# Kernel tuning notes

Measured on AMD Instinct MI355X. Metric: run time of the kernel, lower is better.

Reference implementation:

```python
import jax, jax.numpy as jnp
import numpy as np

B, C, D_IN, D_H, D_QK = 64, 512, 1024, 1024, 512
EPS = 1e-5


def setup_inputs() -> dict:
    key = jax.random.key(0)
    ks = jax.random.split(key, 24)
    din2 = D_IN + D_H  # concat([x, h]) feature dim
    s_qk = 1.0 / np.sqrt(din2)
    inp = {
        "x": jax.random.normal(ks[0], (B, C, D_IN), jnp.float32),
        "h": jax.random.normal(ks[1], (B, C, D_H), jnp.float32),
    }
    i = 2
    for g in ("r", "z", "n"):
        inp[f"Wq_{g}"] = jax.random.normal(ks[i], (din2, D_QK), jnp.float32) * s_qk; i += 1
        inp[f"bq_{g}"] = jnp.zeros((D_QK,), jnp.float32)
        inp[f"Wk_{g}"] = jax.random.normal(ks[i], (din2, D_QK), jnp.float32) * s_qk; i += 1
        inp[f"bk_{g}"] = jnp.zeros((D_QK,), jnp.float32)
        inp[f"Wv_{g}"] = jax.random.normal(ks[i], (din2, D_H), jnp.float32) * s_qk; i += 1
        inp[f"bv_{g}"] = jnp.zeros((D_H,), jnp.float32)
    inp["gamma"] = jnp.ones((D_H,), jnp.float32)
    inp["beta"] = jnp.zeros((D_H,), jnp.float32)
    return inp


def _self_attention(xin, Wq, bq, Wk, bk, Wv, bv):
    # xin: (B, C, 2D) ; attention over channel axis C
    Q = xin @ Wq + bq            # (B, C, d_qk)
    K = xin @ Wk + bk            # (B, C, d_qk)
    V = xin @ Wv + bv            # (B, C, d_h)
    scale = 1.0 / jnp.sqrt(jnp.asarray(Q.shape[-1], jnp.float32))
    scores = jnp.einsum("bcd,bed->bce", Q, K) * scale   # (B, C, C)
    attn = jax.nn.softmax(scores, axis=-1)
    return jnp.einsum("bce,bed->bcd", attn, V)          # (B, C, d_h)


def reference(x, h,
              Wq_r, bq_r, Wk_r, bk_r, Wv_r, bv_r,
              Wq_z, bq_z, Wk_z, bk_z, Wv_z, bv_z,
              Wq_n, bq_n, Wk_n, bk_n, Wv_n, bv_n,
              gamma, beta):
    xh = jnp.concatenate([x, h], axis=2)
    r = _self_attention(xh, Wq_r, bq_r, Wk_r, bk_r, Wv_r, bv_r)
    z = _self_attention(xh, Wq_z, bq_z, Wk_z, bk_z, Wv_z, bv_z)
    reset = jax.nn.sigmoid(r)
    update = jax.nn.sigmoid(z)
    xhr = jnp.concatenate([x, h * reset], axis=2)
    n = _self_attention(xhr, Wq_n, bq_n, Wk_n, bk_n, Wv_n, bv_n)
    new_state = (1.0 - update) * h + update * jnp.tanh(n)
    # LayerNorm over last dim
    mu = jnp.mean(new_state, axis=-1, keepdims=True)
    var = jnp.var(new_state, axis=-1, keepdims=True)
    return (new_state - mu) * jax.lax.rsqrt(var + EPS) * gamma + beta
```

## Files before the change

kernel.cpp:

```cpp
#include <hip/hip_runtime.h>
#include <math.h>

typedef __attribute__((ext_vector_type(8))) short short8;
typedef __attribute__((ext_vector_type(4))) float f32x4;

#define EPI_BF16   0
#define EPI_SCORES 1
#define EPI_R      2
#define EPI_Z      3
#define EPI_N      4

__device__ __forceinline__ unsigned short f2bf(float f) {
    unsigned int u = __float_as_uint(f);
    u += 0x7fffu + ((u >> 16) & 1u);
    return (unsigned short)(u >> 16);
}
__device__ __forceinline__ float bf2f(unsigned short s) {
    return __uint_as_float(((unsigned int)s) << 16);
}

struct alignas(8) us4 { unsigned short a, b, c, d; };

#define GLD_LDS16(gp, lp) \
    __builtin_amdgcn_global_load_lds((const __attribute__((address_space(1))) unsigned int*)(gp), \
                                     (__attribute__((address_space(3))) unsigned int*)(lp), 16, 0, 0)

#define BAR   do { asm volatile("" ::: "memory"); __builtin_amdgcn_s_barrier(); \
                   asm volatile("" ::: "memory"); } while (0)
#define VMC4  asm volatile("s_waitcnt vmcnt(4)" ::: "memory")
#define VMC0  asm volatile("s_waitcnt vmcnt(0)" ::: "memory")

template<int EPI, int SWZ>
__global__ void __launch_bounds__(512, 2)
gemm256(const unsigned short* __restrict__ A, long long sAb, int lda,
        const unsigned short* __restrict__ Bt, long long sBb, int ldb,
        const float* __restrict__ bias,
        void* __restrict__ C, long long sCb, int ldc,
        int K, float scale,
        const float* __restrict__ hptr,
        const unsigned short* __restrict__ updptr)
{
    extern __shared__ char smem[];

    const int z = blockIdx.z;
    A  += (size_t)z * (size_t)sAb;
    Bt += (size_t)z * (size_t)sBb;

    int bx, by;
    if (SWZ) {
        const int bid = blockIdx.y * 8 + blockIdx.x;
        const int xcd = bid & 7, i = bid >> 3;
        bx = i & 7;
        by = (xcd << 4) | (i >> 3);
    } else {
        bx = blockIdx.x; by = blockIdx.y;
    }
    const int m0 = by * 256;
    const int n0 = bx * 256;

    const int tid = threadIdx.x;
    const int w  = tid >> 6;
    const int l  = tid & 63;
    const int wr = w >> 2;
    const int wc = w & 3;
    const int lr = l & 15;
    const int lg = l >> 4;
    const int rs = (lr & 7) << 4;

    const int srw = l >> 3;
    const int scb = ((l & 7) << 4) ^ (srw << 4);

    const long long ldab = (long long)lda * 2;
    const long long ldbb = (long long)ldb * 2;

    f32x4 acc[2][4][4] = {};
    short8 a[4][2], b[4][2];

#define STAGE1(gbase, ldbytes, grow0, ldsoff) { \
    const char* g_ = (const char*)(gbase) + \
        (size_t)((grow0) + w*8 + srw) * (ldbytes) + scb; \
    GLD_LDS16(g_, smem + (ldsoff) + (w << 10)); }

#define AOFF(buf) ((buf)*65536)
#define BOFF(buf) ((buf)*65536 + 32768)

#define STAGE_A0(kt, buf) { STAGE1(A, ldab, m0 + 0   + 0*0, AOFF(buf) + 0);      \
                            STAGE1(A + (size_t)(kt)*0, ldab, m0 + 128, AOFF(buf) + 16384); } (void)0
#define STAGE_B0(kt, buf) { STAGE1(Bt, ldbb, n0 + 0,   BOFF(buf) + 0);      \
                            STAGE1(Bt, ldbb, n0 + 128, BOFF(buf) + 16384); } (void)0
#define STAGE_A1(kt, buf) { STAGE1(A, ldab, m0 + 64,  AOFF(buf) + 8192);  \
                            STAGE1(A, ldab, m0 + 192, AOFF(buf) + 24576); } (void)0
#define STAGE_B1(kt, buf) { STAGE1(Bt, ldbb, n0 + 64,  BOFF(buf) + 8192);  \
                            STAGE1(Bt, ldbb, n0 + 192, BOFF(buf) + 24576); } (void)0

#define LDA8(MH, buf) { \
    const char* Ab_ = smem + AOFF(buf); \
    _Pragma("unroll") \
    for (int mf = 0; mf < 4; ++mf) { \
        const int row_ = wr*128 + (MH)*64 + mf*16 + lr; \
        _Pragma("unroll") \
        for (int kk = 0; kk < 2; ++kk) \
            a[mf][kk] = *(const short8*)(Ab_ + row_*128 + ((kk*64 + lg*16) ^ rs)); } }

#define LDB4(BH, buf) { \
    const char* Bb_ = smem + BOFF(buf); \
    _Pragma("unroll") \
    for (int nf = 0; nf < 2; ++nf) { \
        const int row_ = wc*64 + (BH)*32 + nf*16 + lr; \
        _Pragma("unroll") \
        for (int kk = 0; kk < 2; ++kk) \
            b[(BH)*2+nf][kk] = *(const short8*)(Bb_ + row_*128 + ((kk*64 + lg*16) ^ rs)); } }

#define MMA16(MH, BH) { \
    __builtin_amdgcn_s_setprio(1); \
    _Pragma("unroll") \
    for (int kk = 0; kk < 2; ++kk) \
    _Pragma("unroll") \
    for (int mf = 0; mf < 4; ++mf) \
    _Pragma("unroll") \
    for (int nf = 0; nf < 2; ++nf) \
        acc[MH][mf][(BH)*2+nf] = __builtin_amdgcn_mfma_f32_16x16x32_bf16( \
            a[mf][kk], b[(BH)*2+nf][kk], acc[MH][mf][(BH)*2+nf], 0, 0, 0); \
    __builtin_amdgcn_s_setprio(0); }

    {
        const unsigned short* A0p = A;           const unsigned short* B0p = Bt;
        (void)A0p; (void)B0p;
        { const long long kb = 0;
          STAGE1(A  + (kb>>1), ldab, m0 + 0,   AOFF(0) + 0);
          STAGE1(A  + (kb>>1), ldab, m0 + 128, AOFF(0) + 16384);
          STAGE1(A  + (kb>>1), ldab, m0 + 64,  AOFF(0) + 8192);
          STAGE1(A  + (kb>>1), ldab, m0 + 192, AOFF(0) + 24576);
          STAGE1(Bt + (kb>>1), ldbb, n0 + 0,   BOFF(0) + 0);
          STAGE1(Bt + (kb>>1), ldbb, n0 + 128, BOFF(0) + 16384);
          STAGE1(Bt + (kb>>1), ldbb, n0 + 64,  BOFF(0) + 8192);
          STAGE1(Bt + (kb>>1), ldbb, n0 + 192, BOFF(0) + 24576); }
        { const long long kb = 128;
          STAGE1(A  + (kb>>1), ldab, m0 + 0,   AOFF(1) + 0);
          STAGE1(A  + (kb>>1), ldab, m0 + 128, AOFF(1) + 16384);
          STAGE1(A  + (kb>>1), ldab, m0 + 64,  AOFF(1) + 8192);
          STAGE1(A  + (kb>>1), ldab, m0 + 192, AOFF(1) + 24576); }
        VMC4;
        BAR;
    }

    const int NT = K >> 6;
    for (int t = 0; t < NT; ++t) {
        const int p = t & 1, q = p ^ 1;
        const unsigned short* An = A  + (size_t)(t + 2) * 64;
        const unsigned short* Bn = Bt + (size_t)(t + 1) * 64;
        const bool sB = (t + 1 < NT), sA = (t + 2 < NT);

        LDA8(0, p); LDB4(0, p);
        if (sB) { STAGE1(Bn, ldbb, n0 + 0,   BOFF(q) + 0);
                  STAGE1(Bn, ldbb, n0 + 128, BOFF(q) + 16384); }
        BAR;
        MMA16(0, 0);
        LDB4(1, p);
        if (sB) { STAGE1(Bn, ldbb, n0 + 64,  BOFF(q) + 8192);
                  STAGE1(Bn, ldbb, n0 + 192, BOFF(q) + 24576); }
        BAR;
        MMA16(0, 1);
        LDA8(1, p);
        if (sA) { STAGE1(An, ldab, m0 + 0,   AOFF(p) + 0);
                  STAGE1(An, ldab, m0 + 128, AOFF(p) + 16384); }
        BAR;
        MMA16(1, 1);
        BAR;
        if (sA) { STAGE1(An, ldab, m0 + 64,  AOFF(p) + 8192);
                  STAGE1(An, ldab, m0 + 192, AOFF(p) + 24576);
                  VMC4; }
        else if (sB) { VMC0; }
        BAR;
        MMA16(1, 0);
    }

    const int Mb = gridDim.y << 8;
    const size_t zc = (size_t)z * (size_t)sCb;
    #pragma unroll
    for (int mh = 0; mh < 2; ++mh) {
        #pragma unroll
        for (int mf = 0; mf < 4; ++mf) {
            #pragma unroll
            for (int nf = 0; nf < 4; ++nf) {
                const int col = n0 + wc * 64 + nf * 16 + lr;
                const float bval = (EPI == EPI_BF16) ? bias[col] : 0.0f;
                #pragma unroll
                for (int r = 0; r < 4; ++r) {
                    const int row = m0 + wr * 128 + mh * 64 + mf * 16 + lg * 4 + r;
                    float v = acc[mh][mf][nf][r] + bval;
                    if (EPI == EPI_BF16) {
                        ((unsigned short*)C)[zc + (size_t)row * ldc + col] = f2bf(v);
                    } else if (EPI == EPI_SCORES) {
                        ((float*)C)[zc + (size_t)row * ldc + col] = v * scale;
                    } else if (EPI == EPI_R) {
                        const size_t flat = (size_t)z * Mb + row;
                        const float hh = hptr[flat * 1024 + col];
                        const float sg = 1.0f / (1.0f + __expf(-v));
                        ((unsigned short*)C)[flat * 2048 + 1024 + col] = f2bf(hh * sg);
                    } else if (EPI == EPI_Z) {
                        const size_t flat = (size_t)z * Mb + row;
                        const float sg = 1.0f / (1.0f + __expf(-v));
                        ((unsigned short*)C)[flat * 1024 + col] = f2bf(sg);
                    } else {
                        const size_t flat = (size_t)z * Mb + row;
                        const float u  = bf2f(updptr[flat * 1024 + col]);
                        const float hh = hptr[flat * 1024 + col];
                        ((float*)C)[flat * 1024 + col] = (1.0f - u) * hh + u * tanhf(v);
                    }
                }
            }
        }
    }
#undef STAGE1
#undef AOFF
#undef BOFF
#undef STAGE_A0
#undef STAGE_A1
#undef STAGE_B0
#undef STAGE_B1
#undef LDA8
#undef LDB4
#undef MMA16
}


__global__ void __launch_bounds__(256)
prep_xh(const float* __restrict__ x, const float* __restrict__ h, unsigned short* __restrict__ xh)
{
    const size_t t = (size_t)blockIdx.x * 256 + threadIdx.x;
    const size_t f = t * 4;
    const size_t row = f >> 10, col = f & 1023;
    const float4 vx = *(const float4*)(x + f);
    const float4 vh = *(const float4*)(h + f);
    us4 ox = { f2bf(vx.x), f2bf(vx.y), f2bf(vx.z), f2bf(vx.w) };
    us4 oh = { f2bf(vh.x), f2bf(vh.y), f2bf(vh.z), f2bf(vh.w) };
    *(us4*)(xh + row * 2048 + col)        = ox;
    *(us4*)(xh + row * 2048 + 1024 + col) = oh;
}

__global__ void __launch_bounds__(256)
transpose_w(const float* __restrict__ W, unsigned short* __restrict__ WT, int N)
{
    __shared__ float t[32][33];
    const int k0 = blockIdx.y * 32, n0 = blockIdx.x * 32;
    const int tx = threadIdx.x & 31, ty = threadIdx.x >> 5;
    #pragma unroll
    for (int i = 0; i < 4; ++i)
        t[ty + i * 8][tx] = W[(size_t)(k0 + ty + i * 8) * N + n0 + tx];
    __syncthreads();
    #pragma unroll
    for (int i = 0; i < 4; ++i)
        WT[(size_t)(n0 + ty + i * 8) * 2048 + k0 + tx] = f2bf(t[tx][ty + i * 8]);
}

__global__ void __launch_bounds__(256)
transpose_v(const unsigned short* __restrict__ V, unsigned short* __restrict__ Vt)
{
    __shared__ unsigned short t[32][34];
    const int z = blockIdx.z;
    const unsigned short* in = V + (size_t)z * 512 * 2048;
    unsigned short* outp = Vt + (size_t)z * 1024 * 512;
    const int c0 = blockIdx.x * 32, r0 = blockIdx.y * 32;
    const int tx = threadIdx.x & 31, ty = threadIdx.x >> 5;
    #pragma unroll
    for (int i = 0; i < 4; ++i)
        t[ty + i * 8][tx] = in[(size_t)(r0 + ty + i * 8) * 2048 + c0 + tx];
    __syncthreads();
    #pragma unroll
    for (int i = 0; i < 4; ++i)
        outp[(size_t)(c0 + ty + i * 8) * 512 + r0 + tx] = t[tx][ty + i * 8];
}

__global__ void __launch_bounds__(256)
softmax512(const float* __restrict__ S, unsigned short* __restrict__ P)
{
    const int row = blockIdx.x * 4 + (threadIdx.x >> 6);
    const int l = threadIdx.x & 63;
    const float* s = S + (size_t)row * 512;
    const float4 v0 = ((const float4*)s)[l];
    const float4 v1 = ((const float4*)s)[64 + l];
    float m = fmaxf(fmaxf(fmaxf(v0.x, v0.y), fmaxf(v0.z, v0.w)),
                    fmaxf(fmaxf(v1.x, v1.y), fmaxf(v1.z, v1.w)));
    #pragma unroll
    for (int d = 32; d; d >>= 1) m = fmaxf(m, __shfl_xor(m, d));
    float e0 = __expf(v0.x - m), e1 = __expf(v0.y - m), e2 = __expf(v0.z - m), e3 = __expf(v0.w - m);
    float e4 = __expf(v1.x - m), e5 = __expf(v1.y - m), e6 = __expf(v1.z - m), e7 = __expf(v1.w - m);
    float sum = e0 + e1 + e2 + e3 + e4 + e5 + e6 + e7;
    #pragma unroll
    for (int d = 32; d; d >>= 1) sum += __shfl_xor(sum, d);
    const float inv = 1.0f / sum;
    unsigned short* p = P + (size_t)row * 512;
    us4 aa = { f2bf(e0 * inv), f2bf(e1 * inv), f2bf(e2 * inv), f2bf(e3 * inv) };
    us4 bb = { f2bf(e4 * inv), f2bf(e5 * inv), f2bf(e6 * inv), f2bf(e7 * inv) };
    ((us4*)p)[l] = aa;
    ((us4*)p)[64 + l] = bb;
}

__global__ void __launch_bounds__(256)
layernorm1024(float* __restrict__ Y, const float* __restrict__ gamma, const float* __restrict__ beta)
{
    const int row = blockIdx.x * 4 + (threadIdx.x >> 6);
    const int l = threadIdx.x & 63;
    float* p = Y + (size_t)row * 1024;
    float4 v[4];
    float s = 0.0f, s2 = 0.0f;
    #pragma unroll
    for (int i = 0; i < 4; ++i) {
        v[i] = ((const float4*)p)[i * 64 + l];
        s  += v[i].x + v[i].y + v[i].z + v[i].w;
        s2 += v[i].x * v[i].x + v[i].y * v[i].y + v[i].z * v[i].z + v[i].w * v[i].w;
    }
    #pragma unroll
    for (int d = 32; d; d >>= 1) { s += __shfl_xor(s, d); s2 += __shfl_xor(s2, d); }
    const float mu = s * (1.0f / 1024.0f);
    const float var = s2 * (1.0f / 1024.0f) - mu * mu;
    const float inv = rsqrtf(var + 1e-5f);
    #pragma unroll
    for (int i = 0; i < 4; ++i) {
        const float4 gv = ((const float4*)gamma)[i * 64 + l];
        const float4 bv = ((const float4*)beta)[i * 64 + l];
        float4 o;
        o.x = (v[i].x - mu) * inv * gv.x + bv.x;
        o.y = (v[i].y - mu) * inv * gv.y + bv.y;
        o.z = (v[i].z - mu) * inv * gv.z + bv.z;
        o.w = (v[i].w - mu) * inv * gv.w + bv.w;
        ((float4*)p)[i * 64 + l] = o;
    }
}

__global__ void __launch_bounds__(256)
concat_bias(const float* __restrict__ a, const float* __restrict__ b,
            const float* __restrict__ c, float* __restrict__ o)
{
    const int i = blockIdx.x * 256 + threadIdx.x;
    o[i] = (i < 512) ? a[i] : (i < 1024) ? b[i - 512] : c[i - 1024];
}

extern "C" void kernel_launch(void* const* d_in, const int* in_sizes, int n_in,
                              void* d_out, int out_size, void* d_ws, size_t ws_size,
                              hipStream_t stream)
{
    (void)in_sizes; (void)n_in; (void)out_size; (void)ws_size;

    const float* x = (const float*)d_in[0];
    const float* h = (const float*)d_in[1];
    const float* Wf[9]; const float* bia[9];
    for (int g = 0; g < 3; ++g)
        for (int j = 0; j < 3; ++j) {
            Wf[g * 3 + j]  = (const float*)d_in[2 + g * 6 + j * 2];
            bia[g * 3 + j] = (const float*)d_in[2 + g * 6 + j * 2 + 1];
        }
    const float* gamma = (const float*)d_in[20];
    const float* beta  = (const float*)d_in[21];
    float* out = (float*)d_out;

    const int LDS_BYTES = 131072;
    hipFuncSetAttribute((const void*)gemm256<EPI_BF16, 1>,   hipFuncAttributeMaxDynamicSharedMemorySize, LDS_BYTES);
    hipFuncSetAttribute((const void*)gemm256<EPI_SCORES, 0>, hipFuncAttributeMaxDynamicSharedMemorySize, LDS_BYTES);
    hipFuncSetAttribute((const void*)gemm256<EPI_R, 0>,      hipFuncAttributeMaxDynamicSharedMemorySize, LDS_BYTES);
    hipFuncSetAttribute((const void*)gemm256<EPI_Z, 0>,      hipFuncAttributeMaxDynamicSharedMemorySize, LDS_BYTES);
    hipFuncSetAttribute((const void*)gemm256<EPI_N, 0>,      hipFuncAttributeMaxDynamicSharedMemorySize, LDS_BYTES);

    char* ws = (char*)d_ws;
    size_t off = 0;
    auto alloc = [&](size_t bytes) -> void* {
        void* p = ws + off; off += (bytes + 255) & ~(size_t)255; return p;
    };
    unsigned short* xh  = (unsigned short*)alloc((size_t)32768 * 2048 * 2);
    unsigned short* WT  = (unsigned short*)alloc((size_t)12582912 * 2);
    unsigned short* QKV = (unsigned short*)alloc((size_t)32768 * 2048 * 2);
    unsigned short* Vt  = (unsigned short*)alloc((size_t)32768 * 1024 * 2);
    float*          Sc  = (float*)alloc((size_t)64 * 512 * 512 * 4);
    unsigned short* Pb  = (unsigned short*)alloc((size_t)64 * 512 * 512 * 2);
    unsigned short* upd = (unsigned short*)alloc((size_t)32768 * 1024 * 2);
    float*          bct = (float*)alloc((size_t)3 * 2048 * 4);

    size_t wtoff[9];
    {
        size_t o = 0;
        for (int g = 0; g < 3; ++g) {
            wtoff[g * 3 + 0] = o; o += (size_t)512 * 2048;
            wtoff[g * 3 + 1] = o; o += (size_t)512 * 2048;
            wtoff[g * 3 + 2] = o; o += (size_t)1024 * 2048;
        }
    }

    prep_xh<<<32768, 256, 0, stream>>>(x, h, xh);
    for (int i = 0; i < 9; ++i) {
        const int N = (i % 3 == 2) ? 1024 : 512;
        transpose_w<<<dim3(N / 32, 64, 1), 256, 0, stream>>>(Wf[i], WT + wtoff[i], N);
    }
    for (int g = 0; g < 3; ++g)
        concat_bias<<<8, 256, 0, stream>>>(bia[g * 3 + 0], bia[g * 3 + 1], bia[g * 3 + 2], bct + g * 2048);

    const float scscale = 0.044194173824159216f;

    auto gate = [&](int g, int epi) {
        const unsigned short* wT = WT + wtoff[g * 3 + 0];
        gemm256<EPI_BF16, 1><<<dim3(8, 128, 1), 512, LDS_BYTES, stream>>>(
            xh, 0, 2048, wT, 0, 2048, bct + g * 2048, QKV, 0, 2048, 2048, 0.0f, nullptr, nullptr);
        transpose_v<<<dim3(32, 16, 64), 256, 0, stream>>>(QKV + 1024, Vt);
        gemm256<EPI_SCORES, 0><<<dim3(2, 2, 64), 512, LDS_BYTES, stream>>>(
            QKV, 1048576, 2048, QKV + 512, 1048576, 2048, nullptr,
            Sc, 262144, 512, 512, scscale, nullptr, nullptr);
        softmax512<<<8192, 256, 0, stream>>>(Sc, Pb);
        if (epi == EPI_Z)
            gemm256<EPI_Z, 0><<<dim3(4, 2, 64), 512, LDS_BYTES, stream>>>(
                Pb, 262144, 512, Vt, 524288, 512, nullptr, upd, 0, 1024, 512, 0.0f, nullptr, nullptr);
        else if (epi == EPI_R)
            gemm256<EPI_R, 0><<<dim3(4, 2, 64), 512, LDS_BYTES, stream>>>(
                Pb, 262144, 512, Vt, 524288, 512, nullptr, xh, 0, 2048, 512, 0.0f, h, nullptr);
        else
            gemm256<EPI_N, 0><<<dim3(4, 2, 64), 512, LDS_BYTES, stream>>>(
                Pb, 262144, 512, Vt, 524288, 512, nullptr, out, 0, 1024, 512, 0.0f, h, upd);
    };

    gate(1, EPI_Z);
    gate(0, EPI_R);
    gate(2, EPI_N);
    layernorm1024<<<8192, 256, 0, stream>>>(out, gamma, beta);
}
```

Baseline: 1.407 ms.

## Fuse softmax exp into score GEMM, V transpose into QKV epilogue, defer normalization

The score GEMM epilogue now writes exp(scaled score) as bf16 together with per-block row partial sums, and the PV GEMM epilogue divides by the summed partials. This removes the fp32 score buffer, the separate softmax kernel and its max-subtraction pass. The QKV GEMM writes V directly in transposed layout, which removes the transpose_v kernel. Skipping the max subtraction risks overflow for large scores and changes bf16 rounding of the unnormalized probabilities.

```diff
diff --git a/kernel.cpp b/kernel.cpp
--- a/kernel.cpp
+++ b/kernel.cpp
@@ -4,11 +4,11 @@
 typedef __attribute__((ext_vector_type(8))) short short8;
 typedef __attribute__((ext_vector_type(4))) float f32x4;
 
-#define EPI_BF16   0
-#define EPI_SCORES 1
-#define EPI_R      2
-#define EPI_Z      3
-#define EPI_N      4
+#define EPI_QKV   0
+#define EPI_PEXP  1
+#define EPI_R     2
+#define EPI_Z     3
+#define EPI_N     4
 
 __device__ __forceinline__ unsigned short f2bf(float f) {
     unsigned int u = __float_as_uint(f);
@@ -38,7 +38,9 @@
         void* __restrict__ C, long long sCb, int ldc,
         int K, float scale,
         const float* __restrict__ hptr,
-        const unsigned short* __restrict__ updptr)
+        const unsigned short* __restrict__ updptr,
+        float* __restrict__ psum,
+        unsigned short* __restrict__ vt)
 {
     extern __shared__ char smem[];
 
@@ -83,15 +85,6 @@
 
 #define AOFF(buf) ((buf)*65536)
 #define BOFF(buf) ((buf)*65536 + 32768)
-
-#define STAGE_A0(kt, buf) { STAGE1(A, ldab, m0 + 0   + 0*0, AOFF(buf) + 0);      \
-                            STAGE1(A + (size_t)(kt)*0, ldab, m0 + 128, AOFF(buf) + 16384); } (void)0
-#define STAGE_B0(kt, buf) { STAGE1(Bt, ldbb, n0 + 0,   BOFF(buf) + 0);      \
-                            STAGE1(Bt, ldbb, n0 + 128, BOFF(buf) + 16384); } (void)0
-#define STAGE_A1(kt, buf) { STAGE1(A, ldab, m0 + 64,  AOFF(buf) + 8192);  \
-                            STAGE1(A, ldab, m0 + 192, AOFF(buf) + 24576); } (void)0
-#define STAGE_B1(kt, buf) { STAGE1(Bt, ldbb, n0 + 64,  BOFF(buf) + 8192);  \
-                            STAGE1(Bt, ldbb, n0 + 192, BOFF(buf) + 24576); } (void)0
 
 #define LDA8(MH, buf) { \
     const char* Ab_ = smem + AOFF(buf); \
@@ -124,22 +117,18 @@
     __builtin_amdgcn_s_setprio(0); }
 
     {
-        const unsigned short* A0p = A;           const unsigned short* B0p = Bt;
-        (void)A0p; (void)B0p;
-        { const long long kb = 0;
-          STAGE1(A  + (kb>>1), ldab, m0 + 0,   AOFF(0) + 0);
-          STAGE1(A  + (kb>>1), ldab, m0 + 128, AOFF(0) + 16384);
-          STAGE1(A  + (kb>>1), ldab, m0 + 64,  AOFF(0) + 8192);
-          STAGE1(A  + (kb>>1), ldab, m0 + 192, AOFF(0) + 24576);
-          STAGE1(Bt + (kb>>1), ldbb, n0 + 0,   BOFF(0) + 0);
-          STAGE1(Bt + (kb>>1), ldbb, n0 + 128, BOFF(0) + 16384);
-          STAGE1(Bt + (kb>>1), ldbb, n0 + 64,  BOFF(0) + 8192);
-          STAGE1(Bt + (kb>>1), ldbb, n0 + 192, BOFF(0) + 24576); }
-        { const long long kb = 128;
-          STAGE1(A  + (kb>>1), ldab, m0 + 0,   AOFF(1) + 0);
-          STAGE1(A  + (kb>>1), ldab, m0 + 128, AOFF(1) + 16384);
-          STAGE1(A  + (kb>>1), ldab, m0 + 64,  AOFF(1) + 8192);
-          STAGE1(A  + (kb>>1), ldab, m0 + 192, AOFF(1) + 24576); }
+        STAGE1(A,        ldab, m0 + 0,   AOFF(0) + 0);
+        STAGE1(A,        ldab, m0 + 128, AOFF(0) + 16384);
+        STAGE1(A,        ldab, m0 + 64,  AOFF(0) + 8192);
+        STAGE1(A,        ldab, m0 + 192, AOFF(0) + 24576);
+        STAGE1(Bt,       ldbb, n0 + 0,   BOFF(0) + 0);
+        STAGE1(Bt,       ldbb, n0 + 128, BOFF(0) + 16384);
+        STAGE1(Bt,       ldbb, n0 + 64,  BOFF(0) + 8192);
+        STAGE1(Bt,       ldbb, n0 + 192, BOFF(0) + 24576);
+        STAGE1(A + 64,   ldab, m0 + 0,   AOFF(1) + 0);
+        STAGE1(A + 64,   ldab, m0 + 128, AOFF(1) + 16384);
+        STAGE1(A + 64,   ldab, m0 + 64,  AOFF(1) + 8192);
+        STAGE1(A + 64,   ldab, m0 + 192, AOFF(1) + 24576);
         VMC4;
         BAR;
     }
@@ -177,36 +166,115 @@
 
     const int Mb = gridDim.y << 8;
     const size_t zc = (size_t)z * (size_t)sCb;
-    #pragma unroll
-    for (int mh = 0; mh < 2; ++mh) {
-        #pragma unroll
-        for (int mf = 0; mf < 4; ++mf) {
-            #pragma unroll
-            for (int nf = 0; nf < 4; ++nf) {
-                const int col = n0 + wc * 64 + nf * 16 + lr;
-                const float bval = (EPI == EPI_BF16) ? bias[col] : 0.0f;
+
+    if (EPI == EPI_PEXP) {
+        float psl[2][4][4];
+        #pragma unroll
+        for (int mh = 0; mh < 2; ++mh)
+            #pragma unroll
+            for (int mf = 0; mf < 4; ++mf)
+                #pragma unroll
+                for (int r = 0; r < 4; ++r) psl[mh][mf][r] = 0.0f;
+
+        #pragma unroll
+        for (int mh = 0; mh < 2; ++mh)
+        #pragma unroll
+        for (int mf = 0; mf < 4; ++mf)
+        #pragma unroll
+        for (int nf = 0; nf < 4; ++nf) {
+            const int col = n0 + wc * 64 + nf * 16 + lr;
+            #pragma unroll
+            for (int r = 0; r < 4; ++r) {
+                const int row = m0 + wr * 128 + mh * 64 + mf * 16 + lg * 4 + r;
+                const float e = __expf(acc[mh][mf][nf][r] * scale);
+                ((unsigned short*)C)[zc + (size_t)row * ldc + col] = f2bf(e);
+                psl[mh][mf][r] += e;
+            }
+        }
+        #pragma unroll
+        for (int d = 1; d < 16; d <<= 1)
+            #pragma unroll
+            for (int mh = 0; mh < 2; ++mh)
+                #pragma unroll
+                for (int mf = 0; mf < 4; ++mf)
+                    #pragma unroll
+                    for (int r = 0; r < 4; ++r)
+                        psl[mh][mf][r] += __shfl_xor(psl[mh][mf][r], d);
+        __syncthreads();
+        float* red = (float*)smem;
+        if (lr == 0) {
+            #pragma unroll
+            for (int mh = 0; mh < 2; ++mh)
+                #pragma unroll
+                for (int mf = 0; mf < 4; ++mf)
+                    #pragma unroll
+                    for (int r = 0; r < 4; ++r)
+                        red[wc * 256 + wr * 128 + mh * 64 + mf * 16 + lg * 4 + r]
+                            = psl[mh][mf][r];
+        }
+        __syncthreads();
+        if (tid < 256) {
+            const float sres = red[tid] + red[256 + tid] + red[512 + tid] + red[768 + tid];
+            psum[(size_t)bx * 32768 + (size_t)z * 512 + m0 + tid] = sres;
+        }
+        return;
+    }
+
+    float invs[2][4][4];
+    if (EPI == EPI_R || EPI == EPI_Z || EPI == EPI_N) {
+        #pragma unroll
+        for (int mh = 0; mh < 2; ++mh)
+            #pragma unroll
+            for (int mf = 0; mf < 4; ++mf)
                 #pragma unroll
                 for (int r = 0; r < 4; ++r) {
                     const int row = m0 + wr * 128 + mh * 64 + mf * 16 + lg * 4 + r;
-                    float v = acc[mh][mf][nf][r] + bval;
-                    if (EPI == EPI_BF16) {
-                        ((unsigned short*)C)[zc + (size_t)row * ldc + col] = f2bf(v);
-                    } else if (EPI == EPI_SCORES) {
-                        ((float*)C)[zc + (size_t)row * ldc + col] = v * scale;
-                    } else if (EPI == EPI_R) {
-                        const size_t flat = (size_t)z * Mb + row;
-                        const float hh = hptr[flat * 1024 + col];
-                        const float sg = 1.0f / (1.0f + __expf(-v));
-                        ((unsigned short*)C)[flat * 2048 + 1024 + col] = f2bf(hh * sg);
-                    } else if (EPI == EPI_Z) {
-                        const size_t flat = (size_t)z * Mb + row;
-                        const float sg = 1.0f / (1.0f + __expf(-v));
-                        ((unsigned short*)C)[flat * 1024 + col] = f2bf(sg);
-                    } else {
-                        const size_t flat = (size_t)z * Mb + row;
-                        const float u  = bf2f(updptr[flat * 1024 + col]);
-                        const float hh = hptr[flat * 1024 + col];
-                        ((float*)C)[flat * 1024 + col] = (1.0f - u) * hh + u * tanhf(v);
+                    const size_t gr = (size_t)z * 512 + row;
+                    invs[mh][mf][r] = 1.0f / (psum[gr] + psum[32768 + gr]);
+                }
+    }
+
+    #pragma unroll
+    for (int mh = 0; mh < 2; ++mh) {
+        #pragma unroll
+        for (int mf = 0; mf < 4; ++mf) {
+            #pragma unroll
+            for (int nf = 0; nf < 4; ++nf) {
+                const int col = n0 + wc * 64 + nf * 16 + lr;
+                const float bval = (EPI == EPI_QKV) ? bias[col] : 0.0f;
+                if (EPI == EPI_QKV && bx >= 4) {
+                    const int row0 = m0 + wr * 128 + mh * 64 + mf * 16 + lg * 4;
+                    us4 o = { f2bf(acc[mh][mf][nf][0] + bval),
+                              f2bf(acc[mh][mf][nf][1] + bval),
+                              f2bf(acc[mh][mf][nf][2] + bval),
+                              f2bf(acc[mh][mf][nf][3] + bval) };
+                    *(us4*)(vt + (size_t)(row0 >> 9) * 524288 +
+                            (size_t)(col - 1024) * 512 + (row0 & 511)) = o;
+                } else {
+                    #pragma unroll
+                    for (int r = 0; r < 4; ++r) {
+                        const int row = m0 + wr * 128 + mh * 64 + mf * 16 + lg * 4 + r;
+                        float v = acc[mh][mf][nf][r] + bval;
+                        if (EPI == EPI_QKV) {
+                            ((unsigned short*)C)[(size_t)row * ldc + col] = f2bf(v);
+                        } else if (EPI == EPI_R) {
+                            v *= invs[mh][mf][r];
+                            const size_t flat = (size_t)z * Mb + row;
+                            const float hh = hptr[flat * 1024 + col];
+                            const float sg = 1.0f / (1.0f + __expf(-v));
+                            ((unsigned short*)C)[flat * 2048 + 1024 + col] = f2bf(hh * sg);
+                        } else if (EPI == EPI_Z) {
+                            v *= invs[mh][mf][r];
+                            const size_t flat = (size_t)z * Mb + row;
+                            const float sg = 1.0f / (1.0f + __expf(-v));
+                            ((unsigned short*)C)[flat * 1024 + col] = f2bf(sg);
+                        } else {
+                            v *= invs[mh][mf][r];
+                            const size_t flat = (size_t)z * Mb + row;
+                            const float u  = bf2f(updptr[flat * 1024 + col]);
+                            const float hh = hptr[flat * 1024 + col];
+                            ((float*)C)[flat * 1024 + col] = (1.0f - u) * hh + u * tanhf(v);
+                        }
                     }
                 }
             }
@@ -215,10 +283,6 @@
 #undef STAGE1
 #undef AOFF
 #undef BOFF
-#undef STAGE_A0
-#undef STAGE_A1
-#undef STAGE_B0
-#undef STAGE_B1
 #undef LDA8
 #undef LDB4
 #undef MMA16
@@ -255,49 +319,6 @@
 }
 
 __global__ void __launch_bounds__(256)
-transpose_v(const unsigned short* __restrict__ V, unsigned short* __restrict__ Vt)
-{
-    __shared__ unsigned short t[32][34];
-    const int z = blockIdx.z;
-    const unsigned short* in = V + (size_t)z * 512 * 2048;
-    unsigned short* outp = Vt + (size_t)z * 1024 * 512;
-    const int c0 = blockIdx.x * 32, r0 = blockIdx.y * 32;
-    const int tx = threadIdx.x & 31, ty = threadIdx.x >> 5;
-    #pragma unroll
-    for (int i = 0; i < 4; ++i)
-        t[ty + i * 8][tx] = in[(size_t)(r0 + ty + i * 8) * 2048 + c0 + tx];
-    __syncthreads();
-    #pragma unroll
-    for (int i = 0; i < 4; ++i)
-        outp[(size_t)(c0 + ty + i * 8) * 512 + r0 + tx] = t[tx][ty + i * 8];
-}
-
-__global__ void __launch_bounds__(256)
-softmax512(const float* __restrict__ S, unsigned short* __restrict__ P)
-{
-    const int row = blockIdx.x * 4 + (threadIdx.x >> 6);
-    const int l = threadIdx.x & 63;
-    const float* s = S + (size_t)row * 512;
-    const float4 v0 = ((const float4*)s)[l];
-    const float4 v1 = ((const float4*)s)[64 + l];
-    float m = fmaxf(fmaxf(fmaxf(v0.x, v0.y), fmaxf(v0.z, v0.w)),
-                    fmaxf(fmaxf(v1.x, v1.y), fmaxf(v1.z, v1.w)));
-    #pragma unroll
-    for (int d = 32; d; d >>= 1) m = fmaxf(m, __shfl_xor(m, d));
-    float e0 = __expf(v0.x - m), e1 = __expf(v0.y - m), e2 = __expf(v0.z - m), e3 = __expf(v0.w - m);
-    float e4 = __expf(v1.x - m), e5 = __expf(v1.y - m), e6 = __expf(v1.z - m), e7 = __expf(v1.w - m);
-    float sum = e0 + e1 + e2 + e3 + e4 + e5 + e6 + e7;
-    #pragma unroll
-    for (int d = 32; d; d >>= 1) sum += __shfl_xor(sum, d);
-    const float inv = 1.0f / sum;
-    unsigned short* p = P + (size_t)row * 512;
-    us4 aa = { f2bf(e0 * inv), f2bf(e1 * inv), f2bf(e2 * inv), f2bf(e3 * inv) };
-    us4 bb = { f2bf(e4 * inv), f2bf(e5 * inv), f2bf(e6 * inv), f2bf(e7 * inv) };
-    ((us4*)p)[l] = aa;
-    ((us4*)p)[64 + l] = bb;
-}
-
-__global__ void __launch_bounds__(256)
 layernorm1024(float* __restrict__ Y, const float* __restrict__ gamma, const float* __restrict__ beta)
 {
     const int row = blockIdx.x * 4 + (threadIdx.x >> 6);
@@ -356,11 +377,11 @@
     float* out = (float*)d_out;
 
     const int LDS_BYTES = 131072;
-    hipFuncSetAttribute((const void*)gemm256<EPI_BF16, 1>,   hipFuncAttributeMaxDynamicSharedMemorySize, LDS_BYTES);
-    hipFuncSetAttribute((const void*)gemm256<EPI_SCORES, 0>, hipFuncAttributeMaxDynamicSharedMemorySize, LDS_BYTES);
-    hipFuncSetAttribute((const void*)gemm256<EPI_R, 0>,      hipFuncAttributeMaxDynamicSharedMemorySize, LDS_BYTES);
-    hipFuncSetAttribute((const void*)gemm256<EPI_Z, 0>,      hipFuncAttributeMaxDynamicSharedMemorySize, LDS_BYTES);
-    hipFuncSetAttribute((const void*)gemm256<EPI_N, 0>,      hipFuncAttributeMaxDynamicSharedMemorySize, LDS_BYTES);
+    hipFuncSetAttribute((const void*)gemm256<EPI_QKV, 1>,  hipFuncAttributeMaxDynamicSharedMemorySize, LDS_BYTES);
+    hipFuncSetAttribute((const void*)gemm256<EPI_PEXP, 0>, hipFuncAttributeMaxDynamicSharedMemorySize, LDS_BYTES);
+    hipFuncSetAttribute((const void*)gemm256<EPI_R, 0>,    hipFuncAttributeMaxDynamicSharedMemorySize, LDS_BYTES);
+    hipFuncSetAttribute((const void*)gemm256<EPI_Z, 0>,    hipFuncAttributeMaxDynamicSharedMemorySize, LDS_BYTES);
+    hipFuncSetAttribute((const void*)gemm256<EPI_N, 0>,    hipFuncAttributeMaxDynamicSharedMemorySize, LDS_BYTES);
 
     char* ws = (char*)d_ws;
     size_t off = 0;
@@ -369,11 +390,11 @@
     };
     unsigned short* xh  = (unsigned short*)alloc((size_t)32768 * 2048 * 2);
     unsigned short* WT  = (unsigned short*)alloc((size_t)12582912 * 2);
-    unsigned short* QKV = (unsigned short*)alloc((size_t)32768 * 2048 * 2);
+    unsigned short* QK  = (unsigned short*)alloc((size_t)32768 * 1024 * 2);
     unsigned short* Vt  = (unsigned short*)alloc((size_t)32768 * 1024 * 2);
-    float*          Sc  = (float*)alloc((size_t)64 * 512 * 512 * 4);
     unsigned short* Pb  = (unsigned short*)alloc((size_t)64 * 512 * 512 * 2);
     unsigned short* upd = (unsigned short*)alloc((size_t)32768 * 1024 * 2);
+    float*          psb = (float*)alloc((size_t)2 * 32768 * 4);
     float*          bct = (float*)alloc((size_t)3 * 2048 * 4);
 
     size_t wtoff[9];
@@ -398,22 +419,24 @@
 
     auto gate = [&](int g, int epi) {
         const unsigned short* wT = WT + wtoff[g * 3 + 0];
-        gemm256<EPI_BF16, 1><<<dim3(8, 128, 1), 512, LDS_BYTES, stream>>>(
-            xh, 0, 2048, wT, 0, 2048, bct + g * 2048, QKV, 0, 2048, 2048, 0.0f, nullptr, nullptr);
-        transpose_v<<<dim3(32, 16, 64), 256, 0, stream>>>(QKV + 1024, Vt);
-        gemm256<EPI_SCORES, 0><<<dim3(2, 2, 64), 512, LDS_BYTES, stream>>>(
-            QKV, 1048576, 2048, QKV + 512, 1048576, 2048, nullptr,
-            Sc, 262144, 512, 512, scscale, nullptr, nullptr);
-        softmax512<<<8192, 256, 0, stream>>>(Sc, Pb);
+        gemm256<EPI_QKV, 1><<<dim3(8, 128, 1), 512, LDS_BYTES, stream>>>(
+            xh, 0, 2048, wT, 0, 2048, bct + g * 2048,
+            QK, 0, 1024, 2048, 0.0f, nullptr, nullptr, nullptr, Vt);
+        gemm256<EPI_PEXP, 0><<<dim3(2, 2, 64), 512, LDS_BYTES, stream>>>(
+            QK, 524288, 1024, QK + 512, 524288, 1024, nullptr,
+            Pb, 262144, 512, 512, scscale, nullptr, nullptr, psb, nullptr);
         if (epi == EPI_Z)
             gemm256<EPI_Z, 0><<<dim3(4, 2, 64), 512, LDS_BYTES, stream>>>(
-                Pb, 262144, 512, Vt, 524288, 512, nullptr, upd, 0, 1024, 512, 0.0f, nullptr, nullptr);
+                Pb, 262144, 512, Vt, 524288, 512, nullptr,
+                upd, 0, 1024, 512, 0.0f, nullptr, nullptr, psb, nullptr);
         else if (epi == EPI_R)
             gemm256<EPI_R, 0><<<dim3(4, 2, 64), 512, LDS_BYTES, stream>>>(
-                Pb, 262144, 512, Vt, 524288, 512, nullptr, xh, 0, 2048, 512, 0.0f, h, nullptr);
+                Pb, 262144, 512, Vt, 524288, 512, nullptr,
+                xh, 0, 2048, 512, 0.0f, h, nullptr, psb, nullptr);
         else
             gemm256<EPI_N, 0><<<dim3(4, 2, 64), 512, LDS_BYTES, stream>>>(
-                Pb, 262144, 512, Vt, 524288, 512, nullptr, out, 0, 1024, 512, 0.0f, h, upd);
+                Pb, 262144, 512, Vt, 524288, 512, nullptr,
+                out, 0, 1024, 512, 0.0f, h, upd, psb, nullptr);
     };
 
     gate(1, EPI_Z);
```

Measured after the change: 1.295 ms. 1.09x faster.
